# Optimization experiments

Measured on AMD Instinct MI355X. Metric: run time of the kernel, lower is better.

The kernel has to match this reference:

```python
import jax, jax.numpy as jnp
import numpy as np

N_NODES = 100000
N_EDGES = 1600000
IN_DIM, HID_DIM, OUT_DIM = 32, 64, 8


def sage_conv(x, src, dst, W_l, b_l, W_r, n_nodes):
    # PyG SAGEConv (aggr='mean', root_weight=True):
    # out_i = W_l @ mean_{j in N(i)} x_j + b_l + W_r @ x_i
    msg_sum = jax.ops.segment_sum(x[src], dst, num_segments=n_nodes)  # [N, F]
    deg = jax.ops.segment_sum(jnp.ones((src.shape[0],), x.dtype), dst,
                              num_segments=n_nodes)  # [N]
    agg = msg_sum / jnp.maximum(deg, 1.0)[:, None]
    return agg @ W_l.T + b_l + x @ W_r.T


def setup_inputs() -> dict:
    key = jax.random.key(0)
    ks = jax.random.split(key, 8)
    x = jax.random.normal(ks[0], (N_NODES, IN_DIM), dtype=jnp.float32)
    edge_index = jax.random.randint(ks[1], (2, N_EDGES), 0, N_NODES, dtype=jnp.int64)
    s1 = 1.0 / np.sqrt(IN_DIM)
    s2 = 1.0 / np.sqrt(HID_DIM)
    return {
        "x": x,
        "edge_index": edge_index,
        "W1_l": jax.random.uniform(ks[2], (HID_DIM, IN_DIM), jnp.float32, -s1, s1),
        "b1": jnp.zeros((HID_DIM,), jnp.float32),
        "W1_r": jax.random.uniform(ks[3], (HID_DIM, IN_DIM), jnp.float32, -s1, s1),
        "W2_l": jax.random.uniform(ks[4], (OUT_DIM, HID_DIM), jnp.float32, -s2, s2),
        "b2": jnp.zeros((OUT_DIM,), jnp.float32),
        "W2_r": jax.random.uniform(ks[5], (OUT_DIM, HID_DIM), jnp.float32, -s2, s2),
    }


def reference(x, edge_index, W1_l, b1, W1_r, W2_l, b2, W2_r):
    src, dst = edge_index[0], edge_index[1]
    h = sage_conv(x, src, dst, W1_l, b1, W1_r, N_NODES)
    h = jax.nn.relu(h)
    out = sage_conv(h, src, dst, W2_l, b2, W2_r, N_NODES)
    return out
```

## Files before the change

### kernel.cpp

```cpp
#include <hip/hip_runtime.h>

#define N_NODES 100000
#define N_EDGES 1600000
#define IN_DIM 32
#define HID_DIM 64
#define OUT_DIM 8
#define CAP 64
#define CHUNK 4096
#define NCHUNK ((N_EDGES + CHUNK - 1) / CHUNK)
#define SLICE_W (N_NODES / 8)
#define QCAP 262144

typedef unsigned short u16;
typedef unsigned int u32;
typedef unsigned long long ull;

__device__ __forceinline__ float bf2f(u16 v) {
    return __uint_as_float(((u32)v) << 16);
}

__device__ __forceinline__ u16 f2bf(float f) {
    u32 u = __float_as_uint(f);
    u32 lsb = (u >> 16) & 1u;
    u += 0x7fffu + lsb;
    return (u16)(u >> 16);
}

__device__ __forceinline__ float ldf(const void* p, size_t i, int bf) {
    return bf ? bf2f(((const u16*)p)[i]) : ((const float*)p)[i];
}

__global__ __launch_bounds__(256) void k_prep(
    const int* __restrict__ ei, const u32* __restrict__ xw,
    const void* __restrict__ W1l, const void* __restrict__ b1,
    const void* __restrict__ W1r,
    const void* __restrict__ W2l, const void* __restrict__ b2,
    const void* __restrict__ W2r,
    int* __restrict__ flags,
    float* __restrict__ tW1l, float* __restrict__ tW1r,
    float* __restrict__ tW2l, float* __restrict__ tW2r,
    float* __restrict__ tb1, float* __restrict__ tb2)
{
    __shared__ int bfs;
    int t = threadIdx.x;
    if (t < 64) {
        int v = ei[2 * t + 1];
        ull m1 = __ballot(v == 0);
        u32 w = xw[t];
        u32 b = (w >> 8) & 0x7fu;
        ull m2 = __ballot(b >= 0x38u && b <= 0x41u);
        if (t == 0) {
            flags[0] = (m1 == ~0ULL) ? 1 : 0;
            int bf = (__popcll(m2) >= 56) ? 1 : 0;
            flags[1] = bf;
            bfs = bf;
        }
    }
    __syncthreads();
    int bf = bfs;
    for (int i = t; i < HID_DIM * IN_DIM; i += 256) {
        int o = i / IN_DIM, k = i % IN_DIM;
        tW1l[k * HID_DIM + o] = ldf(W1l, i, bf);
        tW1r[k * HID_DIM + o] = ldf(W1r, i, bf);
    }
    for (int i = t; i < OUT_DIM * HID_DIM; i += 256) {
        int o = i / HID_DIM, k = i % HID_DIM;
        tW2l[k * OUT_DIM + o] = ldf(W2l, i, bf);
        tW2r[k * OUT_DIM + o] = ldf(W2r, i, bf);
    }
    if (t < HID_DIM) tb1[t] = ldf(b1, t, bf);
    if (t < OUT_DIM) tb2[t] = ldf(b2, t, bf);
}

__global__ __launch_bounds__(256) void k_part(
    const int* __restrict__ ei, const int* __restrict__ flags,
    int* __restrict__ qcnt, u32* __restrict__ qbuf)
{
    __shared__ int hist[4][8], wbase[4][8], lcur[4][8], gbase[8];
    int t = threadIdx.x, w = t >> 6;
    if (t < 32) { hist[t >> 3][t & 7] = 0; lcur[t >> 3][t & 7] = 0; }
    __syncthreads();
    int sh = flags[0];
    int e0 = blockIdx.x * CHUNK;
    int myd[16], mys[16];
    #pragma unroll
    for (int i = 0; i < 16; i++) {
        int e = e0 + i * 256 + t;
        if (e < N_EDGES) {
            size_t off = (size_t)e << sh;
            mys[i] = ei[off];
            int d = ei[((size_t)N_EDGES << sh) + off];
            myd[i] = d;
            atomicAdd(&hist[w][d / SLICE_W], 1);
        } else myd[i] = -1;
    }
    __syncthreads();
    if (t < 8) {
        int tot = hist[0][t] + hist[1][t] + hist[2][t] + hist[3][t];
        gbase[t] = atomicAdd(&qcnt[t], tot);
    }
    __syncthreads();
    if (t < 32) {
        int w2 = t >> 3, s = t & 7;
        int p = gbase[s];
        for (int w3 = 0; w3 < w2; w3++) p += hist[w3][s];
        wbase[w2][s] = p;
    }
    __syncthreads();
    #pragma unroll
    for (int i = 0; i < 16; i++) {
        int d = myd[i];
        if (d >= 0) {
            int s = d / SLICE_W;
            int p = wbase[w][s] + atomicAdd(&lcur[w][s], 1);
            qbuf[(size_t)s * QCAP + p] = ((u32)mys[i] << 14) | (u32)(d - s * SLICE_W);
        }
    }
}

__global__ __launch_bounds__(256) void k_build2(
    const int* __restrict__ qcnt, const u32* __restrict__ qbuf,
    int* __restrict__ cnt, int* __restrict__ slot)
{
    int slice = blockIdx.x & 7, bi = blockIdx.x >> 3;
    int m = qcnt[slice];
    int lo = slice * SLICE_W;
    const u32* q = qbuf + (size_t)slice * QCAP;
    for (int i = bi * 256 + threadIdx.x; i < m; i += 64 * 256) {
        u32 u = q[i];
        int d = lo + (int)(u & 0x3FFFu);
        int s = (int)(u >> 14);
        int pos = atomicAdd(&cnt[d], 1);
        if (pos < CAP) slot[(size_t)d * CAP + pos] = s;
    }
}

__global__ __launch_bounds__(256, 8) void k_sage1(
    const void* __restrict__ x, const int* __restrict__ cnt,
    const int* __restrict__ slot,
    const float* __restrict__ tW1l, const float* __restrict__ tW1r,
    const float* __restrict__ tW2l, const float* __restrict__ tW2r,
    const float* __restrict__ tb1, const float* __restrict__ tb2,
    const int* __restrict__ flags,
    float* __restrict__ gbuf, float* __restrict__ rbuf)
{
    __shared__ float aggbuf[8][IN_DIM];
    __shared__ float xbuf[8][IN_DIM];
    __shared__ float hbuf[8][HID_DIM + 1];

    int t = threadIdx.x;
    int bf = flags[1];
    int wid = t >> 6, lane = t & 63;
    int half = lane >> 5;
    int g2 = (lane >> 3) & 3;
    int l = lane & 7;
    int ns = wid * 2 + half;
    int n = blockIdx.x * 8 + ns;
    int deg = cnt[n];
    int cl = (deg < CAP) ? deg : CAP;
    const int* srow = slot + (size_t)n * CAP;

    float a0 = 0, a1 = 0, a2 = 0, a3 = 0;
    float c0 = 0, c1 = 0, c2 = 0, c3 = 0;
    int j = g2;
    for (; j + 4 < cl; j += 8) {
        int sA = srow[j];
        int sB = srow[j + 4];
        if (bf) {
            ushort4 vA = reinterpret_cast<const ushort4*>((const u16*)x + (size_t)sA * IN_DIM)[l];
            ushort4 vB = reinterpret_cast<const ushort4*>((const u16*)x + (size_t)sB * IN_DIM)[l];
            a0 += bf2f(vA.x); a1 += bf2f(vA.y); a2 += bf2f(vA.z); a3 += bf2f(vA.w);
            c0 += bf2f(vB.x); c1 += bf2f(vB.y); c2 += bf2f(vB.z); c3 += bf2f(vB.w);
        } else {
            float4 vA = reinterpret_cast<const float4*>((const float*)x + (size_t)sA * IN_DIM)[l];
            float4 vB = reinterpret_cast<const float4*>((const float*)x + (size_t)sB * IN_DIM)[l];
            a0 += vA.x; a1 += vA.y; a2 += vA.z; a3 += vA.w;
            c0 += vB.x; c1 += vB.y; c2 += vB.z; c3 += vB.w;
        }
    }
    if (j < cl) {
        int s = srow[j];
        if (bf) {
            ushort4 v = reinterpret_cast<const ushort4*>((const u16*)x + (size_t)s * IN_DIM)[l];
            a0 += bf2f(v.x); a1 += bf2f(v.y); a2 += bf2f(v.z); a3 += bf2f(v.w);
        } else {
            float4 v = reinterpret_cast<const float4*>((const float*)x + (size_t)s * IN_DIM)[l];
            a0 += v.x; a1 += v.y; a2 += v.z; a3 += v.w;
        }
    }
    a0 += c0; a1 += c1; a2 += c2; a3 += c3;
    a0 += __shfl_xor(a0, 8, 64);  a0 += __shfl_xor(a0, 16, 64);
    a1 += __shfl_xor(a1, 8, 64);  a1 += __shfl_xor(a1, 16, 64);
    a2 += __shfl_xor(a2, 8, 64);  a2 += __shfl_xor(a2, 16, 64);
    a3 += __shfl_xor(a3, 8, 64);  a3 += __shfl_xor(a3, 16, 64);
    if (g2 == 0) {
        aggbuf[ns][4 * l + 0] = a0; aggbuf[ns][4 * l + 1] = a1;
        aggbuf[ns][4 * l + 2] = a2; aggbuf[ns][4 * l + 3] = a3;
    } else if (g2 == 1) {
        float f0, f1, f2, f3;
        if (bf) {
            ushort4 v = reinterpret_cast<const ushort4*>((const u16*)x + (size_t)n * IN_DIM)[l];
            f0 = bf2f(v.x); f1 = bf2f(v.y); f2 = bf2f(v.z); f3 = bf2f(v.w);
        } else {
            float4 v = reinterpret_cast<const float4*>((const float*)x + (size_t)n * IN_DIM)[l];
            f0 = v.x; f1 = v.y; f2 = v.z; f3 = v.w;
        }
        xbuf[ns][4 * l + 0] = f0; xbuf[ns][4 * l + 1] = f1;
        xbuf[ns][4 * l + 2] = f2; xbuf[ns][4 * l + 3] = f3;
    }
    __syncthreads();

    float rd0 = 1.0f / fmaxf((float)__shfl(deg, 0, 64), 1.0f);
    float rd1 = 1.0f / fmaxf((float)__shfl(deg, 32, 64), 1.0f);
    int s0 = wid * 2, s1 = wid * 2 + 1;
    int o = lane;
    float bb = tb1[o];
    float acc0 = bb, acc1 = bb;
    #pragma unroll 8
    for (int k = 0; k < IN_DIM; k++) {
        float wl = tW1l[k * HID_DIM + o];
        float wr = tW1r[k * HID_DIM + o];
        acc0 += (aggbuf[s0][k] * rd0) * wl + xbuf[s0][k] * wr;
        acc1 += (aggbuf[s1][k] * rd1) * wl + xbuf[s1][k] * wr;
    }
    hbuf[s0][o] = fmaxf(acc0, 0.0f);
    hbuf[s1][o] = fmaxf(acc1, 0.0f);
    __syncthreads();

    float ga = 0.0f, ra = 0.0f;
    #pragma unroll 4
    for (int m = 0; m < 16; m++) {
        int k = g2 * 16 + m;
        float hv = hbuf[ns][k];
        ga += hv * tW2l[k * OUT_DIM + l];
        ra += hv * tW2r[k * OUT_DIM + l];
    }
    ga += __shfl_xor(ga, 8, 64);  ga += __shfl_xor(ga, 16, 64);
    ra += __shfl_xor(ra, 8, 64);  ra += __shfl_xor(ra, 16, 64);
    if (g2 == 0) {
        gbuf[(size_t)n * OUT_DIM + l] = ga;
        rbuf[(size_t)n * OUT_DIM + l] = ra + tb2[l];
    }
}

__global__ __launch_bounds__(256) void k_sage3(
    const float* __restrict__ gbuf, const float* __restrict__ rbuf,
    const int* __restrict__ cnt, const int* __restrict__ slot,
    const int* __restrict__ flags, void* __restrict__ out)
{
    int t = threadIdx.x;
    int grp = t >> 3, l = t & 7;
    int n = blockIdx.x * 32 + grp;
    int deg = cnt[n];
    int cl = (deg < CAP) ? deg : CAP;
    const int* srow = slot + (size_t)n * CAP;
    float a0 = 0.0f, a1 = 0.0f;
    int j = 0;
    for (; j + 1 < cl; j += 2) {
        int v0 = srow[j];
        int v1 = srow[j + 1];
        a0 += gbuf[(size_t)v0 * OUT_DIM + l];
        a1 += gbuf[(size_t)v1 * OUT_DIM + l];
    }
    if (j < cl) a0 += gbuf[(size_t)srow[j] * OUT_DIM + l];
    float res = (a0 + a1) / fmaxf((float)deg, 1.0f) + rbuf[(size_t)n * OUT_DIM + l];
    size_t oi = (size_t)n * OUT_DIM + l;
    if (flags[1]) ((u16*)out)[oi] = f2bf(res);
    else          ((float*)out)[oi] = res;
}

extern "C" void kernel_launch(void* const* d_in, const int* in_sizes, int n_in,
                              void* d_out, int out_size, void* d_ws, size_t ws_size,
                              hipStream_t stream) {
    const void* x   = d_in[0];
    const int*  ei  = (const int*)d_in[1];
    const void* W1l = d_in[2];
    const void* b1  = d_in[3];
    const void* W1r = d_in[4];
    const void* W2l = d_in[5];
    const void* b2  = d_in[6];
    const void* W2r = d_in[7];

    int* flags   = (int*)d_ws;
    int* cnt     = flags + 4;
    int* qcnt    = cnt + N_NODES;
    float* tW1l  = (float*)(qcnt + 8);
    float* tW1r  = tW1l + IN_DIM * HID_DIM;
    float* tW2l  = tW1r + IN_DIM * HID_DIM;
    float* tW2r  = tW2l + HID_DIM * OUT_DIM;
    float* tb1   = tW2r + HID_DIM * OUT_DIM;
    float* tb2   = tb1 + HID_DIM;
    int* slot    = (int*)(tb2 + OUT_DIM);
    u32* qbuf    = (u32*)(slot + (size_t)N_NODES * CAP);
    float* gbuf  = (float*)(qbuf + (size_t)8 * QCAP);
    float* rbuf  = gbuf + (size_t)N_NODES * OUT_DIM;

    hipMemsetAsync(d_ws, 0, (size_t)(4 + N_NODES + 8) * sizeof(int), stream);

    k_prep<<<1, 256, 0, stream>>>(ei, (const u32*)x, W1l, b1, W1r, W2l, b2, W2r,
                                  flags, tW1l, tW1r, tW2l, tW2r, tb1, tb2);
    k_part<<<NCHUNK, 256, 0, stream>>>(ei, flags, qcnt, qbuf);
    k_build2<<<512, 256, 0, stream>>>(qcnt, qbuf, cnt, slot);
    k_sage1<<<N_NODES / 8, 256, 0, stream>>>(x, cnt, slot, tW1l, tW1r,
                                             tW2l, tW2r, tb1, tb2, flags, gbuf, rbuf);
    k_sage3<<<N_NODES / 32, 256, 0, stream>>>(gbuf, rbuf, cnt, slot, flags, d_out);
}
```

Before: 265.4 us.

## Split layer-1 gather into bf16 feature halves and store layer-2 messages as bf16

Converts x to bf16 and splits it into two 16-feature halves (xlo/xhi) so each layer-1 gather pass reads a 1.6 MB table that may stay cache-resident. The gather is split into two kernels, one per half, with the first half's sums passed through a global buffer. The prep kernel is folded into the partition kernel, which drops a launch and the flags buffer, and the layer-2 message buffer is stored in bf16 with a 4-way unrolled gather. Gathering twice doubles the index reads, adds a launch and an extra buffer round trip, and introduces bf16 rounding when inputs are fp32.

After: 315.8 us. +19.0%, slower.

```diff
diff --git a/kernel.cpp b/kernel.cpp
--- a/kernel.cpp
+++ b/kernel.cpp
@@ -5,9 +5,11 @@
 #define IN_DIM 32
 #define HID_DIM 64
 #define OUT_DIM 8
+#define XH 16
 #define CAP 64
 #define CHUNK 4096
 #define NCHUNK ((N_EDGES + CHUNK - 1) / CHUNK)
+#define RBLK 64
 #define SLICE_W (N_NODES / 8)
 #define QCAP 262144
 
@@ -30,57 +32,61 @@
     return bf ? bf2f(((const u16*)p)[i]) : ((const float*)p)[i];
 }
 
-__global__ __launch_bounds__(256) void k_prep(
+__global__ __launch_bounds__(256) void k_part(
     const int* __restrict__ ei, const u32* __restrict__ xw,
+    const void* __restrict__ x,
     const void* __restrict__ W1l, const void* __restrict__ b1,
     const void* __restrict__ W1r,
     const void* __restrict__ W2l, const void* __restrict__ b2,
     const void* __restrict__ W2r,
-    int* __restrict__ flags,
+    int* __restrict__ qcnt, u32* __restrict__ qbuf,
     float* __restrict__ tW1l, float* __restrict__ tW1r,
     float* __restrict__ tW2l, float* __restrict__ tW2r,
-    float* __restrict__ tb1, float* __restrict__ tb2)
-{
-    __shared__ int bfs;
-    int t = threadIdx.x;
+    float* __restrict__ tb1, float* __restrict__ tb2,
+    u16* __restrict__ xlo, u16* __restrict__ xhi)
+{
+    __shared__ int shv, bfv;
+    __shared__ int hist[4][8], wbase[4][8], lcur[4][8], gbase[8];
+    int t = threadIdx.x, w = t >> 6;
     if (t < 64) {
         int v = ei[2 * t + 1];
         ull m1 = __ballot(v == 0);
-        u32 w = xw[t];
-        u32 b = (w >> 8) & 0x7fu;
+        u32 wd = xw[t];
+        u32 b = (wd >> 8) & 0x7fu;
         ull m2 = __ballot(b >= 0x38u && b <= 0x41u);
         if (t == 0) {
-            flags[0] = (m1 == ~0ULL) ? 1 : 0;
-            int bf = (__popcll(m2) >= 56) ? 1 : 0;
-            flags[1] = bf;
-            bfs = bf;
-        }
-    }
-    __syncthreads();
-    int bf = bfs;
-    for (int i = t; i < HID_DIM * IN_DIM; i += 256) {
-        int o = i / IN_DIM, k = i % IN_DIM;
-        tW1l[k * HID_DIM + o] = ldf(W1l, i, bf);
-        tW1r[k * HID_DIM + o] = ldf(W1r, i, bf);
-    }
-    for (int i = t; i < OUT_DIM * HID_DIM; i += 256) {
-        int o = i / HID_DIM, k = i % HID_DIM;
-        tW2l[k * OUT_DIM + o] = ldf(W2l, i, bf);
-        tW2r[k * OUT_DIM + o] = ldf(W2r, i, bf);
-    }
-    if (t < HID_DIM) tb1[t] = ldf(b1, t, bf);
-    if (t < OUT_DIM) tb2[t] = ldf(b2, t, bf);
-}
-
-__global__ __launch_bounds__(256) void k_part(
-    const int* __restrict__ ei, const int* __restrict__ flags,
-    int* __restrict__ qcnt, u32* __restrict__ qbuf)
-{
-    __shared__ int hist[4][8], wbase[4][8], lcur[4][8], gbase[8];
-    int t = threadIdx.x, w = t >> 6;
+            shv = (m1 == ~0ULL) ? 1 : 0;
+            bfv = (__popcll(m2) >= 56) ? 1 : 0;
+        }
+    }
     if (t < 32) { hist[t >> 3][t & 7] = 0; lcur[t >> 3][t & 7] = 0; }
     __syncthreads();
-    int sh = flags[0];
+    int sh = shv, bf = bfv;
+
+    if (blockIdx.x >= NCHUNK) {
+        for (int i = (blockIdx.x - NCHUNK) * 256 + t; i < N_NODES * XH;
+             i += RBLK * 256) {
+            int node = i >> 4, d = i & 15;
+            xlo[i] = f2bf(ldf(x, (size_t)node * IN_DIM + d, bf));
+            xhi[i] = f2bf(ldf(x, (size_t)node * IN_DIM + XH + d, bf));
+        }
+        return;
+    }
+    if (blockIdx.x == 0) {
+        for (int i = t; i < HID_DIM * IN_DIM; i += 256) {
+            int o = i / IN_DIM, k = i % IN_DIM;
+            tW1l[k * HID_DIM + o] = ldf(W1l, i, bf);
+            tW1r[k * HID_DIM + o] = ldf(W1r, i, bf);
+        }
+        for (int i = t; i < OUT_DIM * HID_DIM; i += 256) {
+            int o = i / HID_DIM, k = i % HID_DIM;
+            tW2l[k * OUT_DIM + o] = ldf(W2l, i, bf);
+            tW2r[k * OUT_DIM + o] = ldf(W2r, i, bf);
+        }
+        if (t < HID_DIM) tb1[t] = ldf(b1, t, bf);
+        if (t < OUT_DIM) tb2[t] = ldf(b2, t, bf);
+    }
+
     int e0 = blockIdx.x * CHUNK;
     int myd[16], mys[16];
     #pragma unroll
@@ -135,21 +141,11 @@
     }
 }
 
-__global__ __launch_bounds__(256, 8) void k_sage1(
-    const void* __restrict__ x, const int* __restrict__ cnt,
-    const int* __restrict__ slot,
-    const float* __restrict__ tW1l, const float* __restrict__ tW1r,
-    const float* __restrict__ tW2l, const float* __restrict__ tW2r,
-    const float* __restrict__ tb1, const float* __restrict__ tb2,
-    const int* __restrict__ flags,
-    float* __restrict__ gbuf, float* __restrict__ rbuf)
-{
-    __shared__ float aggbuf[8][IN_DIM];
-    __shared__ float xbuf[8][IN_DIM];
-    __shared__ float hbuf[8][HID_DIM + 1];
-
+__global__ __launch_bounds__(256, 8) void k_sage1a(
+    const u16* __restrict__ xlo, const int* __restrict__ cnt,
+    const int* __restrict__ slot, float* __restrict__ agglo)
+{
     int t = threadIdx.x;
-    int bf = flags[1];
     int wid = t >> 6, lane = t & 63;
     int half = lane >> 5;
     int g2 = (lane >> 3) & 3;
@@ -160,53 +156,84 @@
     int cl = (deg < CAP) ? deg : CAP;
     const int* srow = slot + (size_t)n * CAP;
 
-    float a0 = 0, a1 = 0, a2 = 0, a3 = 0;
-    float c0 = 0, c1 = 0, c2 = 0, c3 = 0;
+    float a0 = 0, a1 = 0, c0 = 0, c1 = 0;
     int j = g2;
     for (; j + 4 < cl; j += 8) {
         int sA = srow[j];
         int sB = srow[j + 4];
-        if (bf) {
-            ushort4 vA = reinterpret_cast<const ushort4*>((const u16*)x + (size_t)sA * IN_DIM)[l];
-            ushort4 vB = reinterpret_cast<const ushort4*>((const u16*)x + (size_t)sB * IN_DIM)[l];
-            a0 += bf2f(vA.x); a1 += bf2f(vA.y); a2 += bf2f(vA.z); a3 += bf2f(vA.w);
-            c0 += bf2f(vB.x); c1 += bf2f(vB.y); c2 += bf2f(vB.z); c3 += bf2f(vB.w);
-        } else {
-            float4 vA = reinterpret_cast<const float4*>((const float*)x + (size_t)sA * IN_DIM)[l];
-            float4 vB = reinterpret_cast<const float4*>((const float*)x + (size_t)sB * IN_DIM)[l];
-            a0 += vA.x; a1 += vA.y; a2 += vA.z; a3 += vA.w;
-            c0 += vB.x; c1 += vB.y; c2 += vB.z; c3 += vB.w;
-        }
+        ushort2 vA = reinterpret_cast<const ushort2*>(xlo + (size_t)sA * XH)[l];
+        ushort2 vB = reinterpret_cast<const ushort2*>(xlo + (size_t)sB * XH)[l];
+        a0 += bf2f(vA.x); a1 += bf2f(vA.y);
+        c0 += bf2f(vB.x); c1 += bf2f(vB.y);
     }
     if (j < cl) {
         int s = srow[j];
-        if (bf) {
-            ushort4 v = reinterpret_cast<const ushort4*>((const u16*)x + (size_t)s * IN_DIM)[l];
-            a0 += bf2f(v.x); a1 += bf2f(v.y); a2 += bf2f(v.z); a3 += bf2f(v.w);
-        } else {
-            float4 v = reinterpret_cast<const float4*>((const float*)x + (size_t)s * IN_DIM)[l];
-            a0 += v.x; a1 += v.y; a2 += v.z; a3 += v.w;
-        }
-    }
-    a0 += c0; a1 += c1; a2 += c2; a3 += c3;
+        ushort2 v = reinterpret_cast<const ushort2*>(xlo + (size_t)s * XH)[l];
+        a0 += bf2f(v.x); a1 += bf2f(v.y);
+    }
+    a0 += c0; a1 += c1;
     a0 += __shfl_xor(a0, 8, 64);  a0 += __shfl_xor(a0, 16, 64);
     a1 += __shfl_xor(a1, 8, 64);  a1 += __shfl_xor(a1, 16, 64);
-    a2 += __shfl_xor(a2, 8, 64);  a2 += __shfl_xor(a2, 16, 64);
-    a3 += __shfl_xor(a3, 8, 64);  a3 += __shfl_xor(a3, 16, 64);
     if (g2 == 0) {
-        aggbuf[ns][4 * l + 0] = a0; aggbuf[ns][4 * l + 1] = a1;
-        aggbuf[ns][4 * l + 2] = a2; aggbuf[ns][4 * l + 3] = a3;
+        agglo[(size_t)n * XH + 2 * l + 0] = a0;
+        agglo[(size_t)n * XH + 2 * l + 1] = a1;
+    }
+}
+
+__global__ __launch_bounds__(256, 8) void k_sage1b(
+    const u16* __restrict__ xlo, const u16* __restrict__ xhi,
+    const float* __restrict__ agglo,
+    const int* __restrict__ cnt, const int* __restrict__ slot,
+    const float* __restrict__ tW1l, const float* __restrict__ tW1r,
+    const float* __restrict__ tW2l, const float* __restrict__ tW2r,
+    const float* __restrict__ tb1, const float* __restrict__ tb2,
+    u16* __restrict__ gbuf, float* __restrict__ rbuf)
+{
+    __shared__ float aggbuf[8][IN_DIM];
+    __shared__ float xbuf[8][IN_DIM];
+    __shared__ float hbuf[8][HID_DIM + 1];
+
+    int t = threadIdx.x;
+    int wid = t >> 6, lane = t & 63;
+    int half = lane >> 5;
+    int g2 = (lane >> 3) & 3;
+    int l = lane & 7;
+    int ns = wid * 2 + half;
+    int n = blockIdx.x * 8 + ns;
+    int deg = cnt[n];
+    int cl = (deg < CAP) ? deg : CAP;
+    const int* srow = slot + (size_t)n * CAP;
+
+    float a0 = 0, a1 = 0, c0 = 0, c1 = 0;
+    int j = g2;
+    for (; j + 4 < cl; j += 8) {
+        int sA = srow[j];
+        int sB = srow[j + 4];
+        ushort2 vA = reinterpret_cast<const ushort2*>(xhi + (size_t)sA * XH)[l];
+        ushort2 vB = reinterpret_cast<const ushort2*>(xhi + (size_t)sB * XH)[l];
+        a0 += bf2f(vA.x); a1 += bf2f(vA.y);
+        c0 += bf2f(vB.x); c1 += bf2f(vB.y);
+    }
+    if (j < cl) {
+        int s = srow[j];
+        ushort2 v = reinterpret_cast<const ushort2*>(xhi + (size_t)s * XH)[l];
+        a0 += bf2f(v.x); a1 += bf2f(v.y);
+    }
+    a0 += c0; a1 += c1;
+    a0 += __shfl_xor(a0, 8, 64);  a0 += __shfl_xor(a0, 16, 64);
+    a1 += __shfl_xor(a1, 8, 64);  a1 += __shfl_xor(a1, 16, 64);
+    if (g2 == 0) {
+        aggbuf[ns][XH + 2 * l + 0] = a0;
+        aggbuf[ns][XH + 2 * l + 1] = a1;
     } else if (g2 == 1) {
-        float f0, f1, f2, f3;
-        if (bf) {
-            ushort4 v = reinterpret_cast<const ushort4*>((const u16*)x + (size_t)n * IN_DIM)[l];
-            f0 = bf2f(v.x); f1 = bf2f(v.y); f2 = bf2f(v.z); f3 = bf2f(v.w);
-        } else {
-            float4 v = reinterpret_cast<const float4*>((const float*)x + (size_t)n * IN_DIM)[l];
-            f0 = v.x; f1 = v.y; f2 = v.z; f3 = v.w;
-        }
-        xbuf[ns][4 * l + 0] = f0; xbuf[ns][4 * l + 1] = f1;
-        xbuf[ns][4 * l + 2] = f2; xbuf[ns][4 * l + 3] = f3;
+        ushort2 lo = reinterpret_cast<const ushort2*>(xlo + (size_t)n * XH)[l];
+        ushort2 hi = reinterpret_cast<const ushort2*>(xhi + (size_t)n * XH)[l];
+        xbuf[ns][2 * l + 0] = bf2f(lo.x);  xbuf[ns][2 * l + 1] = bf2f(lo.y);
+        xbuf[ns][XH + 2 * l + 0] = bf2f(hi.x);  xbuf[ns][XH + 2 * l + 1] = bf2f(hi.y);
+    } else if (g2 == 2) {
+        float2 v = reinterpret_cast<const float2*>(agglo + (size_t)n * XH)[l];
+        aggbuf[ns][2 * l + 0] = v.x;
+        aggbuf[ns][2 * l + 1] = v.y;
     }
     __syncthreads();
 
@@ -238,35 +265,48 @@
     ga += __shfl_xor(ga, 8, 64);  ga += __shfl_xor(ga, 16, 64);
     ra += __shfl_xor(ra, 8, 64);  ra += __shfl_xor(ra, 16, 64);
     if (g2 == 0) {
-        gbuf[(size_t)n * OUT_DIM + l] = ga;
+        gbuf[(size_t)n * OUT_DIM + l] = f2bf(ga);
         rbuf[(size_t)n * OUT_DIM + l] = ra + tb2[l];
     }
 }
 
 __global__ __launch_bounds__(256) void k_sage3(
-    const float* __restrict__ gbuf, const float* __restrict__ rbuf,
+    const u16* __restrict__ gbuf, const float* __restrict__ rbuf,
     const int* __restrict__ cnt, const int* __restrict__ slot,
-    const int* __restrict__ flags, void* __restrict__ out)
-{
+    const u32* __restrict__ xw, void* __restrict__ out)
+{
+    __shared__ int bfv;
     int t = threadIdx.x;
+    if (t < 64) {
+        u32 w = xw[t];
+        u32 b = (w >> 8) & 0x7fu;
+        ull m2 = __ballot(b >= 0x38u && b <= 0x41u);
+        if (t == 0) bfv = (__popcll(m2) >= 56) ? 1 : 0;
+    }
+    __syncthreads();
     int grp = t >> 3, l = t & 7;
     int n = blockIdx.x * 32 + grp;
     int deg = cnt[n];
     int cl = (deg < CAP) ? deg : CAP;
     const int* srow = slot + (size_t)n * CAP;
-    float a0 = 0.0f, a1 = 0.0f;
+    float a0 = 0.0f, a1 = 0.0f, a2 = 0.0f, a3 = 0.0f;
     int j = 0;
-    for (; j + 1 < cl; j += 2) {
+    for (; j + 3 < cl; j += 4) {
         int v0 = srow[j];
         int v1 = srow[j + 1];
-        a0 += gbuf[(size_t)v0 * OUT_DIM + l];
-        a1 += gbuf[(size_t)v1 * OUT_DIM + l];
-    }
-    if (j < cl) a0 += gbuf[(size_t)srow[j] * OUT_DIM + l];
-    float res = (a0 + a1) / fmaxf((float)deg, 1.0f) + rbuf[(size_t)n * OUT_DIM + l];
+        int v2 = srow[j + 2];
+        int v3 = srow[j + 3];
+        a0 += bf2f(gbuf[(size_t)v0 * OUT_DIM + l]);
+        a1 += bf2f(gbuf[(size_t)v1 * OUT_DIM + l]);
+        a2 += bf2f(gbuf[(size_t)v2 * OUT_DIM + l]);
+        a3 += bf2f(gbuf[(size_t)v3 * OUT_DIM + l]);
+    }
+    for (; j < cl; j++) a0 += bf2f(gbuf[(size_t)srow[j] * OUT_DIM + l]);
+    float res = (a0 + a1 + a2 + a3) / fmaxf((float)deg, 1.0f)
+              + rbuf[(size_t)n * OUT_DIM + l];
     size_t oi = (size_t)n * OUT_DIM + l;
-    if (flags[1]) ((u16*)out)[oi] = f2bf(res);
-    else          ((float*)out)[oi] = res;
+    if (bfv) ((u16*)out)[oi] = f2bf(res);
+    else     ((float*)out)[oi] = res;
 }
 
 extern "C" void kernel_launch(void* const* d_in, const int* in_sizes, int n_in,
@@ -281,8 +321,7 @@
     const void* b2  = d_in[6];
     const void* W2r = d_in[7];
 
-    int* flags   = (int*)d_ws;
-    int* cnt     = flags + 4;
+    int* cnt     = (int*)d_ws;
     int* qcnt    = cnt + N_NODES;
     float* tW1l  = (float*)(qcnt + 8);
     float* tW1r  = tW1l + IN_DIM * HID_DIM;
@@ -292,16 +331,22 @@
     float* tb2   = tb1 + HID_DIM;
     int* slot    = (int*)(tb2 + OUT_DIM);
     u32* qbuf    = (u32*)(slot + (size_t)N_NODES * CAP);
-    float* gbuf  = (float*)(qbuf + (size_t)8 * QCAP);
-    float* rbuf  = gbuf + (size_t)N_NODES * OUT_DIM;
-
-    hipMemsetAsync(d_ws, 0, (size_t)(4 + N_NODES + 8) * sizeof(int), stream);
-
-    k_prep<<<1, 256, 0, stream>>>(ei, (const u32*)x, W1l, b1, W1r, W2l, b2, W2r,
-                                  flags, tW1l, tW1r, tW2l, tW2r, tb1, tb2);
-    k_part<<<NCHUNK, 256, 0, stream>>>(ei, flags, qcnt, qbuf);
+    u16* xlo     = (u16*)(qbuf + (size_t)8 * QCAP);
+    u16* xhi     = xlo + (size_t)N_NODES * XH;
+    float* agglo = (float*)(xhi + (size_t)N_NODES * XH);
+    u16* gbuf    = (u16*)(agglo + (size_t)N_NODES * XH);
+    float* rbuf  = (float*)(gbuf + (size_t)N_NODES * OUT_DIM);
+
+    hipMemsetAsync(d_ws, 0, (size_t)(N_NODES + 8) * sizeof(int), stream);
+
+    k_part<<<NCHUNK + RBLK, 256, 0, stream>>>(
+        ei, (const u32*)x, x, W1l, b1, W1r, W2l, b2, W2r,
+        qcnt, qbuf, tW1l, tW1r, tW2l, tW2r, tb1, tb2, xlo, xhi);
     k_build2<<<512, 256, 0, stream>>>(qcnt, qbuf, cnt, slot);
-    k_sage1<<<N_NODES / 8, 256, 0, stream>>>(x, cnt, slot, tW1l, tW1r,
-                                             tW2l, tW2r, tb1, tb2, flags, gbuf, rbuf);
-    k_sage3<<<N_NODES / 32, 256, 0, stream>>>(gbuf, rbuf, cnt, slot, flags, d_out);
-}
+    k_sage1a<<<N_NODES / 8, 256, 0, stream>>>(xlo, cnt, slot, agglo);
+    k_sage1b<<<N_NODES / 8, 256, 0, stream>>>(xlo, xhi, agglo, cnt, slot,
+                                              tW1l, tW1r, tW2l, tW2r, tb1, tb2,
+                                              gbuf, rbuf);
+    k_sage3<<<N_NODES / 32, 256, 0, stream>>>(gbuf, rbuf, cnt, slot,
+                                              (const u32*)x, d_out);
+}
```
